# Performance work log

Measured on AMD Instinct MI355X. Metric: run time of the kernel, lower is better.

Reference implementation:

```python
import jax, jax.numpy as jnp
import numpy as np

N_MEMBERS = 2      # ensemble_length=3, loop runs i=1..2
N_NODES = 65536    # batch_size * total_length = 32 * 2048
N_EDGES = 1_048_576
N_LAYERS = 12      # num_conv_layers
D = 64             # constant feature width (linspace 64->64)


def setup_inputs() -> dict:
    key = jax.random.key(0)
    k0, k1, k2, k3 = jax.random.split(key, 4)
    x = jax.random.normal(k0, (N_MEMBERS, N_NODES, D), dtype=jnp.float32)
    edge_index = jax.random.randint(k1, (N_MEMBERS, 2, N_EDGES), 0, N_NODES, dtype=jnp.int64)
    # GCNConv weights per member/layer; scale ~ 1/sqrt(D) for stability across 12 layers
    W = jax.random.normal(k2, (N_MEMBERS, N_LAYERS, D, D), dtype=jnp.float32) / jnp.sqrt(jnp.float32(D))
    b = jax.random.normal(k3, (N_MEMBERS, N_LAYERS, D), dtype=jnp.float32) * 0.01
    return {"x": x, "edge_index": edge_index, "W": W, "b": b}


def gcn_conv(h, src, dst, W, b):
    """PyG GCNConv: add self-loops, symmetric D^-1/2 (A+I) D^-1/2 normalization,
    linear transform, bias."""
    hw = h @ W                                                # [N, D_out]
    # degree includes the self-loop (+1)
    deg = jax.ops.segment_sum(jnp.ones((src.shape[0],), h.dtype), dst,
                              num_segments=N_NODES) + jnp.asarray(1.0, h.dtype)
    dinv = jax.lax.rsqrt(deg)                                 # [N]
    norm = dinv[src] * dinv[dst]                              # [E]
    agg = jax.ops.segment_sum(norm[:, None] * hw[src], dst, num_segments=N_NODES)
    agg = agg + (dinv * dinv)[:, None] * hw                   # self-loop term
    return agg + b


def reference(x, edge_index, W, b):
    # eval mode: F.dropout(training=False) is identity
    outs = []
    for i in range(N_MEMBERS):
        src, dst = edge_index[i, 0], edge_index[i, 1]
        h = x[i]
        for j in range(N_LAYERS - 1):
            h = jax.nn.relu(gcn_conv(h, src, dst, W[i, j], b[i, j]))
        outs.append(gcn_conv(h, src, dst, W[i, N_LAYERS - 1], b[i, N_LAYERS - 1]))
    return jnp.stack(outs)  # [N_MEMBERS, N_NODES, D]
```

## Files before the change

kernel.cpp:

```cpp
#include <hip/hip_runtime.h>
#include <hip/hip_fp16.h>
#include <math.h>

#define N_MEMBERS 2
#define N_NODES   65536
#define N_EDGES   1048576
#define N_LAYERS  12
#define D         64
#define OFF_STRIDE (N_NODES + 1)
#define NODE_MASK (N_NODES - 1)

#define NBINS       256
#define BIN_CAP     5120
#define EDGES_PER_WG 4096

typedef _Float16 f16;
typedef f16   f16x8 __attribute__((ext_vector_type(8)));
typedef float f32x4 __attribute__((ext_vector_type(4)));


__global__ __launch_bounds__(256) void bin_scatter_k(const int* __restrict__ ei,
                                                     int* __restrict__ binCursor,
                                                     unsigned int* __restrict__ binned) {
    int m = blockIdx.y;
    int t = threadIdx.x;
    int eBase = blockIdx.x * EDGES_PER_WG;
    __shared__ int hist[NBINS];
    __shared__ int base[NBINS];
    hist[t] = 0;
    __syncthreads();
    const int* srcp = ei + (size_t)(m * 2 + 0) * N_EDGES;
    const int* dstp = ei + (size_t)(m * 2 + 1) * N_EDGES;
    unsigned int pk[16];
    int bn[16], rk[16];
    #pragma unroll
    for (int i = 0; i < 16; i++) {
        int e = eBase + i * 256 + t;
        int src = srcp[e] & NODE_MASK;
        int dst = dstp[e] & NODE_MASK;
        int b = dst >> 8;
        bn[i] = b;
        pk[i] = ((unsigned)src << 8) | (unsigned)(dst & 255);
        rk[i] = atomicAdd(&hist[b], 1);
    }
    __syncthreads();
    base[t] = atomicAdd(&binCursor[m * NBINS + t], hist[t]);
    __syncthreads();
    unsigned int* bb = binned + (size_t)m * NBINS * BIN_CAP;
    #pragma unroll
    for (int i = 0; i < 16; i++) {
        int pos = base[bn[i]] + rk[i];
        if (pos < BIN_CAP)
            bb[(size_t)bn[i] * BIN_CAP + pos] = pk[i];
    }
}

__global__ __launch_bounds__(256) void scan_bins_k(const int* __restrict__ cur,
                                                   int* __restrict__ bbase) {
    int m = blockIdx.x, t = threadIdx.x;
    __shared__ int sh[256];
    int v0 = cur[m * NBINS + t];
    sh[t] = v0;
    __syncthreads();
    for (int ofs = 1; ofs < 256; ofs <<= 1) {
        int v = sh[t];
        int a = (t >= ofs) ? sh[t - ofs] : 0;
        __syncthreads();
        sh[t] = v + a;
        __syncthreads();
    }
    bbase[m * NBINS + t] = sh[t] - v0;
}

__global__ __launch_bounds__(256) void bin_build_k(const unsigned int* __restrict__ binned,
                                                   const int* __restrict__ binCursor,
                                                   const int* __restrict__ bbase,
                                                   int* __restrict__ off,
                                                   float* __restrict__ dinv,
                                                   unsigned short* __restrict__ csr_src) {
    int m = blockIdx.y, b = blockIdx.x, t = threadIdx.x;
    int cnt   = binCursor[m * NBINS + b];
    int gbase = bbase[m * NBINS + b];
    const unsigned int* bb = binned + ((size_t)m * NBINS + b) * BIN_CAP;
    __shared__ int degl[256];
    __shared__ int offl[256];
    degl[t] = 0;
    __syncthreads();
    unsigned int ed[20];
    #pragma unroll
    for (int j = 0; j < 20; j++) {
        int i = t + j * 256;
        ed[j] = 0;
        if (i < cnt) {
            unsigned int w = bb[i];
            int r = atomicAdd(&degl[w & 255], 1);
            ed[j] = w | ((unsigned)r << 24);
        }
    }
    __syncthreads();
    int myDeg = degl[t];
    offl[t] = myDeg;
    __syncthreads();
    for (int ofs = 1; ofs < 256; ofs <<= 1) {
        int v = offl[t];
        int a = (t >= ofs) ? offl[t - ofs] : 0;
        __syncthreads();
        offl[t] = v + a;
        __syncthreads();
    }
    int myOff = gbase + offl[t] - myDeg;
    int node = b * 256 + t;
    off[m * OFF_STRIDE + node] = myOff;
    if (b == NBINS - 1 && t == 255) off[m * OFF_STRIDE + N_NODES] = N_EDGES;
    dinv[m * N_NODES + node] = 1.0f / sqrtf((float)myDeg + 1.0f);
    offl[t] = myOff;
    __syncthreads();
    unsigned short* cs = csr_src + (size_t)m * N_EDGES;
    #pragma unroll
    for (int j = 0; j < 20; j++) {
        int i = t + j * 256;
        if (i < cnt) {
            int dl  = ed[j] & 255;
            int src = (ed[j] >> 8) & 0xFFFF;
            int r   = ed[j] >> 24;
            cs[offl[dl] + r] = (unsigned short)src;
        }
    }
}

__global__ __launch_bounds__(256) void presplit_k(const float* __restrict__ Wall,
                                                  __half* __restrict__ Wsplit) {
    int gid = blockIdx.x * 256 + threadIdx.x;
    int ml   = gid >> 9;
    int r    = gid & 511;
    int t    = (r >> 7) & 3;
    int s    = (r >> 6) & 1;
    int lane = r & 63;
    int c  = t * 16 + (lane & 15);
    int k0 = s * 32 + (lane >> 4) * 8;
    const float* Wg = Wall + (size_t)ml * D * D;
    __half* base = Wsplit + (size_t)ml * 8192;
    int fo = ((t * 2 + s) * 64 + lane) * 8;
    __half hi8[8], lo8[8];
    #pragma unroll
    for (int j = 0; j < 8; j++) {
        float v = Wg[(k0 + j) * D + c];
        f16 h = (f16)v;
        hi8[j] = *(__half*)&h;
        f16 l = (f16)(v - (float)h);
        lo8[j] = *(__half*)&l;
    }
    *(uint4*)(base + fo)        = *(uint4*)hi8;
    *(uint4*)(base + 4096 + fo) = *(uint4*)lo8;
}

__global__ __launch_bounds__(256) void prescale_k(const float* __restrict__ x,
                                                  const float* __restrict__ dinv,
                                                  __half* __restrict__ g) {
    int i = blockIdx.x * 256 + threadIdx.x;
    float dv = dinv[i >> 3];
    float4 a = ((const float4*)x)[i * 2];
    float4 b = ((const float4*)x)[i * 2 + 1];
    union { __half2 h2[4]; uint4 u; } p;
    p.h2[0] = __floats2half2_rn(dv * a.x, dv * a.y);
    p.h2[1] = __floats2half2_rn(dv * a.z, dv * a.w);
    p.h2[2] = __floats2half2_rn(dv * b.x, dv * b.y);
    p.h2[3] = __floats2half2_rn(dv * b.z, dv * b.w);
    ((uint4*)g)[i] = p.u;
}

__device__ __forceinline__ void cvt8(uint4 u, float* f) {
    const __half2* h2 = (const __half2*)&u;
    #pragma unroll
    for (int i = 0; i < 4; i++) {
        float2 t = __half22float2(h2[i]);
        f[2 * i]     = t.x;
        f[2 * i + 1] = t.y;
    }
}

__global__ __launch_bounds__(256) void aggregate_k(const __half* __restrict__ g,
                                                   __half* __restrict__ S,
                                                   const int* __restrict__ off,
                                                   const unsigned short* __restrict__ csr_src,
                                                   const float* __restrict__ dinv) {
    int bflat = blockIdx.x;
    int xcd   = bflat & 7;
    int m     = xcd >> 2;
    int slot  = ((bflat >> 3) << 2) | (xcd & 3);
    int wav   = threadIdx.x >> 6;
    int nA    = slot * 8 + wav * 2;
    int nB    = nA + 1;
    int lane = threadIdx.x & 63;
    int fg   = lane & 7;
    int sub  = lane >> 3;
    const __half*         gm = g + (size_t)m * N_NODES * D;
    const int*            ob = off + m * OFF_STRIDE;
    const unsigned short* sb = csr_src + (size_t)m * N_EDGES;

    float accA[8], accB[8];
    #pragma unroll
    for (int i = 0; i < 8; i++) { accA[i] = 0.f; accB[i] = 0.f; }

    int eA0 = ob[nA], eA1 = ob[nA + 1], eB1 = ob[nB + 1];
    int eB0 = eA1;
    #pragma unroll 2
    for (int eA = eA0, eB = eB0; (eA < eA1) || (eB < eB1); eA += 8, eB += 8) {
        int ia = eA + sub, ib = eB + sub;
        int idxA = (ia < eA1) ? ia : (eA1 - 1);
        int idxB = (ib < eB1) ? ib : (eB1 - 1);
        float wA = (ia < eA1) ? 1.0f : 0.0f;
        float wB = (ib < eB1) ? 1.0f : 0.0f;
        int sA = sb[idxA];
        int sB = sb[idxB];
        uint4 gA = *(const uint4*)(gm + (size_t)sA * D + fg * 8);
        uint4 gB = *(const uint4*)(gm + (size_t)sB * D + fg * 8);
        float fA[8], fB[8];
        cvt8(gA, fA);
        cvt8(gB, fB);
        #pragma unroll
        for (int i = 0; i < 8; i++) {
            accA[i] = fmaf(wA, fA[i], accA[i]);
            accB[i] = fmaf(wB, fB[i], accB[i]);
        }
    }
    #pragma unroll
    for (int msk = 8; msk < 64; msk <<= 1)
        #pragma unroll
        for (int i = 0; i < 8; i++) {
            accA[i] += __shfl_xor(accA[i], msk);
            accB[i] += __shfl_xor(accB[i], msk);
        }

    float dvA = dinv[m * N_NODES + nA];
    float dvB = dinv[m * N_NODES + nB];
    uint4 sgA = *(const uint4*)(gm + (size_t)nA * D + fg * 8);
    uint4 sgB = *(const uint4*)(gm + (size_t)nB * D + fg * 8);
    float sfA[8], sfB[8];
    cvt8(sgA, sfA);
    cvt8(sgB, sfB);
    __half* Sm = S + (size_t)m * N_NODES * D;
    if (sub == 0) {
        union { __half2 h2[4]; uint4 u; } p;
        #pragma unroll
        for (int i = 0; i < 4; i++)
            p.h2[i] = __floats2half2_rn(dvA * (accA[2 * i]     + sfA[2 * i]),
                                        dvA * (accA[2 * i + 1] + sfA[2 * i + 1]));
        *(uint4*)(Sm + (size_t)nA * D + fg * 8) = p.u;
    } else if (sub == 1) {
        union { __half2 h2[4]; uint4 u; } p;
        #pragma unroll
        for (int i = 0; i < 4; i++)
            p.h2[i] = __floats2half2_rn(dvB * (accB[2 * i]     + sfB[2 * i]),
                                        dvB * (accB[2 * i + 1] + sfB[2 * i + 1]));
        *(uint4*)(Sm + (size_t)nB * D + fg * 8) = p.u;
    }
}

__global__ __launch_bounds__(256) void gemm_f16_k(const __half* __restrict__ S,
                                                  const __half* __restrict__ Wsplit,
                                                  const float* __restrict__ dinv,
                                                  const float* __restrict__ ball,
                                                  __half* __restrict__ gout,
                                                  float* __restrict__ fout,
                                                  int layer, int last) {
    int m = blockIdx.y;
    int lane = threadIdx.x & 63;
    int wav  = threadIdx.x >> 6;
    int nn   = lane & 15;
    int quad = lane >> 4;

    const __half* Wf = Wsplit + (size_t)(m * N_LAYERS + layer) * 8192;
    f16x8 Bh[8], Bl[8];
    #pragma unroll
    for (int t = 0; t < 4; t++)
        #pragma unroll
        for (int s = 0; s < 2; s++) {
            int fo = ((t * 2 + s) * 64 + lane) * 8;
            Bh[t * 2 + s] = *(const f16x8*)(Wf + fo);
            Bl[t * 2 + s] = *(const f16x8*)(Wf + 4096 + fo);
        }

    const __half* Sm = S + (size_t)m * N_NODES * D;
    const float*  dm = dinv + m * N_NODES;
    const float*  bp = ball + (size_t)(m * N_LAYERS + layer) * D;
    __half*       gm = gout + (size_t)m * N_NODES * D;
    float*        fm = fout + (size_t)m * N_NODES * D;

    float4 b4[4];
    #pragma unroll
    for (int t = 0; t < 4; t++)
        b4[t] = *(const float4*)(bp + t * 16 + quad * 4);

    int base = blockIdx.x * 128 + wav * 32;
    #pragma unroll
    for (int g = 0; g < 2; g++) {
        int node = base + g * 16 + nn;
        const __half* srow = Sm + (size_t)node * D;
        f16x8 a0 = *(const f16x8*)(srow + quad * 8);
        f16x8 a1 = *(const f16x8*)(srow + 32 + quad * 8);
        float dv = dm[node];
        #pragma unroll
        for (int t = 0; t < 4; t++) {
            f32x4 c = {0.f, 0.f, 0.f, 0.f};
            c = __builtin_amdgcn_mfma_f32_16x16x32_f16(Bh[t * 2 + 0], a0, c, 0, 0, 0);
            c = __builtin_amdgcn_mfma_f32_16x16x32_f16(Bh[t * 2 + 1], a1, c, 0, 0, 0);
            c = __builtin_amdgcn_mfma_f32_16x16x32_f16(Bl[t * 2 + 0], a0, c, 0, 0, 0);
            c = __builtin_amdgcn_mfma_f32_16x16x32_f16(Bl[t * 2 + 1], a1, c, 0, 0, 0);
            float v0 = (float)c[0] + b4[t].x;
            float v1 = (float)c[1] + b4[t].y;
            float v2 = (float)c[2] + b4[t].z;
            float v3 = (float)c[3] + b4[t].w;
            int col = t * 16 + quad * 4;
            if (last) {
                *(float4*)(fm + (size_t)node * D + col) = make_float4(v0, v1, v2, v3);
            } else {
                union { __half2 h2[2]; uint2 u; } p;
                p.h2[0] = __floats2half2_rn(fmaxf(v0, 0.f) * dv, fmaxf(v1, 0.f) * dv);
                p.h2[1] = __floats2half2_rn(fmaxf(v2, 0.f) * dv, fmaxf(v3, 0.f) * dv);
                *(uint2*)(gm + (size_t)node * D + col) = p.u;
            }
        }
    }
}


extern "C" void kernel_launch(void* const* d_in, const int* in_sizes, int n_in,
                              void* d_out, int out_size, void* d_ws, size_t ws_size,
                              hipStream_t stream) {
    (void)in_sizes; (void)n_in; (void)out_size; (void)ws_size;
    const float* x  = (const float*)d_in[0];
    const int*   ei = (const int*)d_in[1];
    const float* W  = (const float*)d_in[2];
    const float* b  = (const float*)d_in[3];
    float* out = (float*)d_out;

    char* ws = (char*)d_ws;
    size_t o = 0;
    auto take = [&](size_t bytes) -> void* {
        void* p = ws + o;
        o = (o + bytes + 255) & ~(size_t)255;
        return p;
    };
    float*          dinv      = (float*) take((size_t)N_MEMBERS * N_NODES * 4);
    int*            off       = (int*)   take((size_t)N_MEMBERS * OFF_STRIDE * 4);
    int*            binCursor = (int*)   take((size_t)N_MEMBERS * NBINS * 4);
    int*            bbase     = (int*)   take((size_t)N_MEMBERS * NBINS * 4);
    unsigned short* csr_src   = (unsigned short*)take((size_t)N_MEMBERS * N_EDGES * 2);
    __half*         Wsplit    = (__half*)take((size_t)N_MEMBERS * N_LAYERS * 8192 * 2);
    __half*         gbuf      = (__half*)take((size_t)N_MEMBERS * N_NODES * D * 2);
    __half*         Sbuf      = (__half*)take((size_t)N_MEMBERS * N_NODES * D * 2);
    unsigned int*   binned    = (unsigned int*)Sbuf;

    hipMemsetAsync(binCursor, 0, (size_t)N_MEMBERS * NBINS * 4, stream);

    presplit_k<<<dim3(N_MEMBERS * N_LAYERS * 512 / 256), 256, 0, stream>>>(W, Wsplit);
    bin_scatter_k<<<dim3(N_EDGES / EDGES_PER_WG, N_MEMBERS), 256, 0, stream>>>(
        ei, binCursor, binned);
    scan_bins_k<<<dim3(N_MEMBERS), 256, 0, stream>>>(binCursor, bbase);
    bin_build_k<<<dim3(NBINS, N_MEMBERS), 256, 0, stream>>>(
        binned, binCursor, bbase, off, dinv, csr_src);
    prescale_k<<<dim3((N_MEMBERS * N_NODES * D / 8) / 256), 256, 0, stream>>>(
        x, dinv, gbuf);

    for (int j = 0; j < N_LAYERS; j++) {
        aggregate_k<<<dim3(N_MEMBERS * (N_NODES / 8)), 256, 0, stream>>>(
            gbuf, Sbuf, off, csr_src, dinv);
        gemm_f16_k<<<dim3(N_NODES / 128, N_MEMBERS), 256, 0, stream>>>(
            Sbuf, Wsplit, dinv, b, gbuf, out, j, (j == N_LAYERS - 1) ? 1 : 0);
    }
}
```

Before: 792.3 us.

## Split GEMM output columns across waves and launch four times more workgroups

```diff
diff --git a/kernel.cpp b/kernel.cpp
--- a/kernel.cpp
+++ b/kernel.cpp
@@ -269,57 +269,53 @@
     int wav  = threadIdx.x >> 6;
     int nn   = lane & 15;
     int quad = lane >> 4;
+    int ng   = wav >> 1;
+    int tp   = wav & 1;
 
     const __half* Wf = Wsplit + (size_t)(m * N_LAYERS + layer) * 8192;
-    f16x8 Bh[8], Bl[8];
-    #pragma unroll
-    for (int t = 0; t < 4; t++)
+    f16x8 Bh[4], Bl[4];
+    #pragma unroll
+    for (int tt = 0; tt < 2; tt++)
         #pragma unroll
         for (int s = 0; s < 2; s++) {
+            int t  = tp * 2 + tt;
             int fo = ((t * 2 + s) * 64 + lane) * 8;
-            Bh[t * 2 + s] = *(const f16x8*)(Wf + fo);
-            Bl[t * 2 + s] = *(const f16x8*)(Wf + 4096 + fo);
+            Bh[tt * 2 + s] = *(const f16x8*)(Wf + fo);
+            Bl[tt * 2 + s] = *(const f16x8*)(Wf + 4096 + fo);
         }
 
     const __half* Sm = S + (size_t)m * N_NODES * D;
-    const float*  dm = dinv + m * N_NODES;
     const float*  bp = ball + (size_t)(m * N_LAYERS + layer) * D;
     __half*       gm = gout + (size_t)m * N_NODES * D;
     float*        fm = fout + (size_t)m * N_NODES * D;
 
-    float4 b4[4];
-    #pragma unroll
-    for (int t = 0; t < 4; t++)
-        b4[t] = *(const float4*)(bp + t * 16 + quad * 4);
-
-    int base = blockIdx.x * 128 + wav * 32;
-    #pragma unroll
-    for (int g = 0; g < 2; g++) {
-        int node = base + g * 16 + nn;
-        const __half* srow = Sm + (size_t)node * D;
-        f16x8 a0 = *(const f16x8*)(srow + quad * 8);
-        f16x8 a1 = *(const f16x8*)(srow + 32 + quad * 8);
-        float dv = dm[node];
-        #pragma unroll
-        for (int t = 0; t < 4; t++) {
-            f32x4 c = {0.f, 0.f, 0.f, 0.f};
-            c = __builtin_amdgcn_mfma_f32_16x16x32_f16(Bh[t * 2 + 0], a0, c, 0, 0, 0);
-            c = __builtin_amdgcn_mfma_f32_16x16x32_f16(Bh[t * 2 + 1], a1, c, 0, 0, 0);
-            c = __builtin_amdgcn_mfma_f32_16x16x32_f16(Bl[t * 2 + 0], a0, c, 0, 0, 0);
-            c = __builtin_amdgcn_mfma_f32_16x16x32_f16(Bl[t * 2 + 1], a1, c, 0, 0, 0);
-            float v0 = (float)c[0] + b4[t].x;
-            float v1 = (float)c[1] + b4[t].y;
-            float v2 = (float)c[2] + b4[t].z;
-            float v3 = (float)c[3] + b4[t].w;
-            int col = t * 16 + quad * 4;
-            if (last) {
-                *(float4*)(fm + (size_t)node * D + col) = make_float4(v0, v1, v2, v3);
-            } else {
-                union { __half2 h2[2]; uint2 u; } p;
-                p.h2[0] = __floats2half2_rn(fmaxf(v0, 0.f) * dv, fmaxf(v1, 0.f) * dv);
-                p.h2[1] = __floats2half2_rn(fmaxf(v2, 0.f) * dv, fmaxf(v3, 0.f) * dv);
-                *(uint2*)(gm + (size_t)node * D + col) = p.u;
-            }
+    int node = blockIdx.x * 32 + ng * 16 + nn;
+    const __half* srow = Sm + (size_t)node * D;
+    f16x8 a0 = *(const f16x8*)(srow + quad * 8);
+    f16x8 a1 = *(const f16x8*)(srow + 32 + quad * 8);
+    float dv = dinv[m * N_NODES + node];
+
+    #pragma unroll
+    for (int tt = 0; tt < 2; tt++) {
+        int t = tp * 2 + tt;
+        f32x4 c = {0.f, 0.f, 0.f, 0.f};
+        c = __builtin_amdgcn_mfma_f32_16x16x32_f16(Bh[tt * 2 + 0], a0, c, 0, 0, 0);
+        c = __builtin_amdgcn_mfma_f32_16x16x32_f16(Bh[tt * 2 + 1], a1, c, 0, 0, 0);
+        c = __builtin_amdgcn_mfma_f32_16x16x32_f16(Bl[tt * 2 + 0], a0, c, 0, 0, 0);
+        c = __builtin_amdgcn_mfma_f32_16x16x32_f16(Bl[tt * 2 + 1], a1, c, 0, 0, 0);
+        float4 b4 = *(const float4*)(bp + t * 16 + quad * 4);
+        float v0 = (float)c[0] + b4.x;
+        float v1 = (float)c[1] + b4.y;
+        float v2 = (float)c[2] + b4.z;
+        float v3 = (float)c[3] + b4.w;
+        int col = t * 16 + quad * 4;
+        if (last) {
+            *(float4*)(fm + (size_t)node * D + col) = make_float4(v0, v1, v2, v3);
+        } else {
+            union { __half2 h2[2]; uint2 u; } p;
+            p.h2[0] = __floats2half2_rn(fmaxf(v0, 0.f) * dv, fmaxf(v1, 0.f) * dv);
+            p.h2[1] = __floats2half2_rn(fmaxf(v2, 0.f) * dv, fmaxf(v3, 0.f) * dv);
+            *(uint2*)(gm + (size_t)node * D + col) = p.u;
         }
     }
 }
@@ -366,7 +362,7 @@
     for (int j = 0; j < N_LAYERS; j++) {
         aggregate_k<<<dim3(N_MEMBERS * (N_NODES / 8)), 256, 0, stream>>>(
             gbuf, Sbuf, off, csr_src, dinv);
-        gemm_f16_k<<<dim3(N_NODES / 128, N_MEMBERS), 256, 0, stream>>>(
+        gemm_f16_k<<<dim3(N_NODES / 32, N_MEMBERS), 256, 0, stream>>>(
             Sbuf, Wsplit, dinv, b, gbuf, out, j, (j == N_LAYERS - 1) ? 1 : 0);
     }
 }
```

Measured after the change: 832.0 us. 5.0% more time.
